# Optimization experiments

Measured on AMD Instinct MI355X. Metric: run time of the kernel, lower is better.

The kernel has to match this reference:

```python
import jax, jax.numpy as jnp
import numpy as np

WS = 7
NHEAD = 8


def setup_inputs() -> dict:
    key = jax.random.key(0)
    k1, k2, k3 = jax.random.split(key, 3)
    B, H, W, D = 32, 56, 56, 256
    x = jax.random.normal(k1, (B, H, W, D), dtype=jnp.float32)
    in_proj_w = jax.random.normal(k2, (3 * D, D), dtype=jnp.float32) * 0.02
    in_proj_b = jnp.zeros((3 * D,), dtype=jnp.float32)
    out_w = jax.random.normal(k3, (D, D), dtype=jnp.float32) * 0.02
    out_b = jnp.zeros((D,), dtype=jnp.float32)
    return {"x": x, "in_proj_w": in_proj_w, "in_proj_b": in_proj_b,
            "out_w": out_w, "out_b": out_b}


def reference(x, in_proj_w, in_proj_b, out_w, out_b):
    B, Hf, Wf, D = x.shape
    ws = WS
    hd = D // NHEAD
    pad_h = (-Hf) % ws
    pad_w = (-Wf) % ws
    xp = jnp.pad(x, ((0, 0), (0, pad_h), (0, pad_w), (0, 0)))
    Hp, Wp = Hf + pad_h, Wf + pad_w
    nh, nw = Hp // ws, Wp // ws
    # partition into windows: [B*nh*nw, ws*ws, D]
    xw = xp.reshape(B, nh, ws, nw, ws, D).transpose(0, 1, 3, 2, 4, 5)
    xw = xw.reshape(B * nh * nw, ws * ws, D)
    N, L = xw.shape[0], ws * ws
    # qkv projection (torch MHA: x @ in_proj_w.T + in_proj_b)
    qkv = jnp.einsum('nld,ed->nle', xw, in_proj_w) + in_proj_b  # [N, L, 3D]
    q, k, v = jnp.split(qkv, 3, axis=-1)
    q = q.reshape(N, L, NHEAD, hd).transpose(0, 2, 1, 3)
    k = k.reshape(N, L, NHEAD, hd).transpose(0, 2, 1, 3)
    v = v.reshape(N, L, NHEAD, hd).transpose(0, 2, 1, 3)
    scale = 1.0 / np.sqrt(hd).astype(np.float32)
    scores = jnp.einsum('nhqd,nhkd->nhqk', q * scale, k)  # [N, H, L, L]
    attn = jax.nn.softmax(scores, axis=-1)
    o = jnp.einsum('nhqk,nhkd->nhqd', attn, v)
    o = o.transpose(0, 2, 1, 3).reshape(N, L, D)
    o = jnp.einsum('nld,ed->nle', o, out_w) + out_b
    # un-window
    o = o.reshape(B, nh, nw, ws, ws, D).transpose(0, 1, 3, 2, 4, 5)
    o = o.reshape(B, Hp, Wp, D)
    return o[:, :Hf, :Wf, :]
```

## Files before the change

kernel.cpp:

```cpp
#include <hip/hip_runtime.h>


using f16   = _Float16;
using f16x4 = __attribute__((ext_vector_type(4))) _Float16;
using f16x8 = __attribute__((ext_vector_type(8))) _Float16;
using f32x4 = __attribute__((ext_vector_type(4))) float;

#define NTOK   100352
#define DMODEL 256
#define QKVN   768
#define QKV_BYTES 154140672ull
#define WQ_HALVES 196608
#define WO_HALVES 65536

typedef const __attribute__((address_space(1))) unsigned int* as1_u32p;
typedef __attribute__((address_space(3))) unsigned int* as3_u32p;

__device__ __forceinline__ void gload16(const void* g, void* l) {
    __builtin_amdgcn_global_load_lds((as1_u32p)g, (as3_u32p)l, 16, 0, 0);
}

__device__ __forceinline__ f16x8 zero8() {
    f16x8 z;
#pragma unroll
    for (int i = 0; i < 8; ++i) z[i] = (f16)0;
    return z;
}

#define WQV4  49152
#define WOV4  16384
__global__ __launch_bounds__(256) void convert_w(
    const float* __restrict__ Wq, const float* __restrict__ Wo,
    f16* __restrict__ Wqh, f16* __restrict__ Woh)
{
    const float scale = 0.17677669529663687f;
    int idx = blockIdx.x * blockDim.x + threadIdx.x;
    if (idx < WQV4) {
        int row = idx >> 6;
        float sc = (row < 256) ? scale : 1.0f;
        float4 f = reinterpret_cast<const float4*>(Wq)[idx];
        f16x4 h;
        h[0]=(f16)(f.x*sc); h[1]=(f16)(f.y*sc); h[2]=(f16)(f.z*sc); h[3]=(f16)(f.w*sc);
        reinterpret_cast<f16x4*>(Wqh)[idx] = h;
    } else if (Woh && idx < WQV4 + WOV4) {
        int j = idx - WQV4;
        float4 f = reinterpret_cast<const float4*>(Wo)[j];
        f16x4 h;
        h[0]=(f16)f.x; h[1]=(f16)f.y; h[2]=(f16)f.z; h[3]=(f16)f.w;
        reinterpret_cast<f16x4*>(Woh)[j] = h;
    }
}

__global__ __launch_bounds__(256) void qkv_gemm(
    const float* __restrict__ X,
    const f16* __restrict__ Wh,
    const float* __restrict__ bias,
    f16* __restrict__ QKV)
{
    __shared__ float As[128 * 64];
    __shared__ f16   Bs[128 * 64];
    const int tid  = threadIdx.x;
    const int lane = tid & 63;
    const int wave = tid >> 6;
    int wg = blockIdx.x;
    const int cpx = (NTOK / 128) * (QKVN / 128) / 8;
    wg = (wg & 7) * cpx + (wg >> 3);
    const int m0 = (wg / (QKVN / 128)) * 128;
    const int n0 = (wg % (QKVN / 128)) * 128;
    const int wm = (wave >> 1) * 64;
    const int wn = (wave & 1) * 64;
    const int g  = lane >> 4;
    const int lr = lane & 15;

    f32x4 acc[4][4] = {};

    for (int k0 = 0; k0 < 256; k0 += 64) {
#pragma unroll
        for (int j = 0; j < 8; ++j) {
            int s   = tid + j * 256;
            int row = s >> 4, c16 = s & 15;
            int cs  = c16 ^ (row & 15);
            gload16(X + (size_t)(m0 + row) * 256 + k0 + cs * 4, &As[s * 4]);
        }
#pragma unroll
        for (int j = 0; j < 4; ++j) {
            int s   = tid + j * 256;
            int row = s >> 3, sl = s & 7;
            int ss  = sl ^ (row & 7);
            gload16(Wh + (size_t)(n0 + row) * 256 + k0 + ss * 8, &Bs[s * 8]);
        }
        __syncthreads();
#pragma unroll
        for (int ks = 0; ks < 2; ++ks) {
            f16x8 a[4], b[4];
#pragma unroll
            for (int i = 0; i < 4; ++i) {
                int row = wm + i * 16 + lr;
                int t0  = (((ks << 2) + g) << 1);
                f32x4 lo = *reinterpret_cast<const f32x4*>(&As[row * 64 + (t0 ^ (row & 15)) * 4]);
                f32x4 hi = *reinterpret_cast<const f32x4*>(&As[row * 64 + ((t0 | 1) ^ (row & 15)) * 4]);
                f16x8 aa;
                aa[0]=(f16)lo[0]; aa[1]=(f16)lo[1]; aa[2]=(f16)lo[2]; aa[3]=(f16)lo[3];
                aa[4]=(f16)hi[0]; aa[5]=(f16)hi[1]; aa[6]=(f16)hi[2]; aa[7]=(f16)hi[3];
                a[i] = aa;
            }
#pragma unroll
            for (int i = 0; i < 4; ++i) {
                int row = wn + i * 16 + lr;
                int c   = ((ks << 2) + g) ^ (row & 7);
                b[i] = *reinterpret_cast<const f16x8*>(&Bs[row * 64 + c * 8]);
            }
#pragma unroll
            for (int mi = 0; mi < 4; ++mi)
#pragma unroll
                for (int ni = 0; ni < 4; ++ni)
                    acc[mi][ni] = __builtin_amdgcn_mfma_f32_16x16x32_f16(a[mi], b[ni], acc[mi][ni], 0, 0, 0);
        }
        __syncthreads();
    }
    const float scale = 0.17677669529663687f;
#pragma unroll
    for (int ni = 0; ni < 4; ++ni) {
        int n = n0 + wn + ni * 16 + lr;
        float bv = bias[n];
        if (n < 256) bv *= scale;
#pragma unroll
        for (int mi = 0; mi < 4; ++mi)
#pragma unroll
            for (int r = 0; r < 4; ++r) {
                int m = m0 + wm + mi * 16 + g * 4 + r;
                QKV[(size_t)m * QKVN + n] = (f16)(acc[mi][ni][r] + bv);
            }
    }
}

__global__ __launch_bounds__(256) void win_attn(f16* __restrict__ QKV)
{
    __shared__ f16 Vt[4][32][68];
    __shared__ f16 P[4][64][68];
    const int tid  = threadIdx.x;
    const int lane = tid & 63;
    const int w    = tid >> 6;
    const int u    = blockIdx.x * 4 + w;
    const int win = u >> 3, h = u & 7;
    const int b = win >> 6, wh = (win >> 3) & 7, ww = win & 7;
    const int base = (b * 56 + wh * 7) * 56 + ww * 7;
    const int g = lane >> 4, lr = lane & 15;

    auto tok = [&](int row) { int rr = row / 7; return base + rr * 56 + (row - rr * 7); };

    f16x8 qf[4], kf[4];
#pragma unroll
    for (int i = 0; i < 4; ++i) {
        int row = i * 16 + lr;
        if (row < 49) {
            size_t off = (size_t)tok(row) * QKVN + h * 32 + g * 8;
            qf[i] = *reinterpret_cast<const f16x8*>(QKV + off);
            kf[i] = *reinterpret_cast<const f16x8*>(QKV + off + 256);
        } else { qf[i] = zero8(); kf[i] = zero8(); }
    }
    {
        int kk = lane;
        if (kk < 49) {
            size_t off = (size_t)tok(kk) * QKVN + 512 + h * 32;
            f16x8 vv[4];
#pragma unroll
            for (int j = 0; j < 4; ++j)
                vv[j] = *reinterpret_cast<const f16x8*>(QKV + off + j * 8);
#pragma unroll
            for (int j = 0; j < 4; ++j)
#pragma unroll
                for (int d = 0; d < 8; ++d) Vt[w][j * 8 + d][kk] = vv[j][d];
        } else {
#pragma unroll
            for (int d = 0; d < 32; ++d) Vt[w][d][kk] = (f16)0;
        }
    }
    f32x4 s[4][4] = {};
#pragma unroll
    for (int ki = 0; ki < 4; ++ki)
#pragma unroll
        for (int qi = 0; qi < 4; ++qi)
            s[ki][qi] = __builtin_amdgcn_mfma_f32_16x16x32_f16(kf[ki], qf[qi], s[ki][qi], 0, 0, 0);

#pragma unroll
    for (int qi = 0; qi < 4; ++qi) {
        float e[4][4];
        float sum = 0.f;
#pragma unroll
        for (int ki = 0; ki < 4; ++ki)
#pragma unroll
            for (int r = 0; r < 4; ++r)
                e[ki][r] = __expf(s[ki][qi][r]);
#pragma unroll
        for (int ki = 0; ki < 3; ++ki)
#pragma unroll
            for (int r = 0; r < 4; ++r)
                sum += e[ki][r];
        sum += (g == 0) ? e[3][0] : 0.f;
        sum += __shfl_xor(sum, 16, 64);
        sum += __shfl_xor(sum, 32, 64);
        float is = 1.f / sum;
#pragma unroll
        for (int ki = 0; ki < 4; ++ki) {
            f16x4 pw;
            pw[0] = (f16)(e[ki][0] * is);
            pw[1] = (f16)(e[ki][1] * is);
            pw[2] = (f16)(e[ki][2] * is);
            pw[3] = (f16)(e[ki][3] * is);
            *reinterpret_cast<f16x4*>(&P[w][qi * 16 + lr][ki * 16 + g * 4]) = pw;
        }
    }
    __syncthreads();

    f32x4 o[4][2] = {};
#pragma unroll
    for (int ks = 0; ks < 2; ++ks) {
        f16x8 pa[4], vb[2];
#pragma unroll
        for (int mi = 0; mi < 4; ++mi)
            pa[mi] = *reinterpret_cast<const f16x8*>(&P[w][mi * 16 + lr][ks * 32 + g * 8]);
#pragma unroll
        for (int ni = 0; ni < 2; ++ni)
            vb[ni] = *reinterpret_cast<const f16x8*>(&Vt[w][ni * 16 + lr][ks * 32 + g * 8]);
#pragma unroll
        for (int mi = 0; mi < 4; ++mi)
#pragma unroll
            for (int ni = 0; ni < 2; ++ni)
                o[mi][ni] = __builtin_amdgcn_mfma_f32_16x16x32_f16(pa[mi], vb[ni], o[mi][ni], 0, 0, 0);
    }
#pragma unroll
    for (int mi = 0; mi < 4; ++mi)
#pragma unroll
        for (int r = 0; r < 4; ++r) {
            int row = mi * 16 + g * 4 + r;
            if (row < 49) {
                size_t off = (size_t)tok(row) * QKVN + h * 32;
#pragma unroll
                for (int ni = 0; ni < 2; ++ni)
                    QKV[off + ni * 16 + lr] = (f16)o[mi][ni][r];
            }
        }
}

__global__ __launch_bounds__(256) void out_gemm_f16(
    const f16* __restrict__ O,
    const f16* __restrict__ Wh,
    const float* __restrict__ bias,
    float* __restrict__ OUT)
{
    __shared__ f16 As[128 * 64];
    __shared__ f16 Bs[128 * 64];
    const int tid  = threadIdx.x;
    const int lane = tid & 63;
    const int wave = tid >> 6;
    int wg = blockIdx.x;
    const int cpx = (NTOK / 128) * (DMODEL / 128) / 8;
    wg = (wg & 7) * cpx + (wg >> 3);
    const int m0 = (wg / (DMODEL / 128)) * 128;
    const int n0 = (wg % (DMODEL / 128)) * 128;
    const int wm = (wave >> 1) * 64;
    const int wn = (wave & 1) * 64;
    const int g  = lane >> 4;
    const int lr = lane & 15;

    f32x4 acc[4][4] = {};

    for (int k0 = 0; k0 < 256; k0 += 64) {
#pragma unroll
        for (int j = 0; j < 4; ++j) {
            int s   = tid + j * 256;
            int row = s >> 3, sl = s & 7;
            int ss  = sl ^ (row & 7);
            gload16(O + (size_t)(m0 + row) * QKVN + k0 + ss * 8, &As[s * 8]);
        }
#pragma unroll
        for (int j = 0; j < 4; ++j) {
            int s   = tid + j * 256;
            int row = s >> 3, sl = s & 7;
            int ss  = sl ^ (row & 7);
            gload16(Wh + (size_t)(n0 + row) * 256 + k0 + ss * 8, &Bs[s * 8]);
        }
        __syncthreads();
#pragma unroll
        for (int ks = 0; ks < 2; ++ks) {
            f16x8 a[4], b[4];
#pragma unroll
            for (int i = 0; i < 4; ++i) {
                int row = wm + i * 16 + lr;
                int c   = ((ks << 2) + g) ^ (row & 7);
                a[i] = *reinterpret_cast<const f16x8*>(&As[row * 64 + c * 8]);
            }
#pragma unroll
            for (int i = 0; i < 4; ++i) {
                int row = wn + i * 16 + lr;
                int c   = ((ks << 2) + g) ^ (row & 7);
                b[i] = *reinterpret_cast<const f16x8*>(&Bs[row * 64 + c * 8]);
            }
#pragma unroll
            for (int mi = 0; mi < 4; ++mi)
#pragma unroll
                for (int ni = 0; ni < 4; ++ni)
                    acc[mi][ni] = __builtin_amdgcn_mfma_f32_16x16x32_f16(a[mi], b[ni], acc[mi][ni], 0, 0, 0);
        }
        __syncthreads();
    }
#pragma unroll
    for (int ni = 0; ni < 4; ++ni) {
        int n = n0 + wn + ni * 16 + lr;
        float bv = bias[n];
#pragma unroll
        for (int mi = 0; mi < 4; ++mi)
#pragma unroll
            for (int r = 0; r < 4; ++r) {
                int m = m0 + wm + mi * 16 + g * 4 + r;
                OUT[(size_t)m * 256 + n] = acc[mi][ni][r] + bv;
            }
    }
}

__global__ __launch_bounds__(256) void out_gemm_cvt(
    const f16* __restrict__ O,
    const float* __restrict__ W,
    const float* __restrict__ bias,
    float* __restrict__ OUT)
{
    __shared__ f16 As[128 * 64];
    __shared__ f16 Bs[128][72];
    const int tid  = threadIdx.x;
    const int lane = tid & 63;
    const int wave = tid >> 6;
    int wg = blockIdx.x;
    const int cpx = (NTOK / 128) * (DMODEL / 128) / 8;
    wg = (wg & 7) * cpx + (wg >> 3);
    const int m0 = (wg / (DMODEL / 128)) * 128;
    const int n0 = (wg % (DMODEL / 128)) * 128;
    const int wm = (wave >> 1) * 64;
    const int wn = (wave & 1) * 64;
    const int g  = lane >> 4;
    const int lr = lane & 15;

    f32x4 acc[4][4] = {};

    for (int k0 = 0; k0 < 256; k0 += 64) {
#pragma unroll
        for (int j = 0; j < 4; ++j) {
            int s   = tid + j * 256;
            int row = s >> 3, sl = s & 7;
            int ss  = sl ^ (row & 7);
            gload16(O + (size_t)(m0 + row) * QKVN + k0 + ss * 8, &As[s * 8]);
        }
#pragma unroll
        for (int j = 0; j < 8; ++j) {
            int v = tid + j * 256;
            int row = v >> 4, cv = v & 15;
            float4 f = *reinterpret_cast<const float4*>(W + (size_t)(n0 + row) * 256 + k0 + cv * 4);
            f16x4 h; h[0]=(f16)f.x; h[1]=(f16)f.y; h[2]=(f16)f.z; h[3]=(f16)f.w;
            *reinterpret_cast<f16x4*>(&Bs[row][cv * 4]) = h;
        }
        __syncthreads();
#pragma unroll
        for (int ks = 0; ks < 2; ++ks) {
            f16x8 a[4], b[4];
#pragma unroll
            for (int i = 0; i < 4; ++i) {
                int row = wm + i * 16 + lr;
                int c   = ((ks << 2) + g) ^ (row & 7);
                a[i] = *reinterpret_cast<const f16x8*>(&As[row * 64 + c * 8]);
            }
#pragma unroll
            for (int i = 0; i < 4; ++i)
                b[i] = *reinterpret_cast<const f16x8*>(&Bs[wn + i * 16 + lr][ks * 32 + g * 8]);
#pragma unroll
            for (int mi = 0; mi < 4; ++mi)
#pragma unroll
                for (int ni = 0; ni < 4; ++ni)
                    acc[mi][ni] = __builtin_amdgcn_mfma_f32_16x16x32_f16(a[mi], b[ni], acc[mi][ni], 0, 0, 0);
        }
        __syncthreads();
    }
#pragma unroll
    for (int ni = 0; ni < 4; ++ni) {
        int n = n0 + wn + ni * 16 + lr;
        float bv = bias[n];
#pragma unroll
        for (int mi = 0; mi < 4; ++mi)
#pragma unroll
            for (int r = 0; r < 4; ++r) {
                int m = m0 + wm + mi * 16 + g * 4 + r;
                OUT[(size_t)m * 256 + n] = acc[mi][ni][r] + bv;
            }
    }
}

extern "C" void kernel_launch(void* const* d_in, const int* in_sizes, int n_in,
                              void* d_out, int out_size, void* d_ws, size_t ws_size,
                              hipStream_t stream) {
    const float* x     = (const float*)d_in[0];
    const float* in_w  = (const float*)d_in[1];
    const float* in_b  = (const float*)d_in[2];
    const float* out_w = (const float*)d_in[3];
    const float* out_b = (const float*)d_in[4];
    float* out = (float*)d_out;
    f16* qkv = (f16*)d_ws;

    const bool tailok = ws_size >= QKV_BYTES + (size_t)(WQ_HALVES + WO_HALVES) * 2;
    f16* wqh = tailok ? (f16*)((char*)d_ws + QKV_BYTES) : (f16*)d_out;
    f16* woh = tailok ? wqh + WQ_HALVES : nullptr;

    convert_w<<<(WQV4 + WOV4 + 255) / 256, 256, 0, stream>>>(in_w, out_w, wqh, woh);

    qkv_gemm<<<(NTOK / 128) * (QKVN / 128), 256, 0, stream>>>(x, wqh, in_b, qkv);

    win_attn<<<4096, 256, 0, stream>>>(qkv);

    if (tailok)
        out_gemm_f16<<<(NTOK / 128) * (DMODEL / 128), 256, 0, stream>>>(qkv, woh, out_b, out);
    else
        out_gemm_cvt<<<(NTOK / 128) * (DMODEL / 128), 256, 0, stream>>>(qkv, out_w, out_b, out);
}
```

Before: 179.9 us.

## Pre-convert X to fp16 and double-buffer the QKV GEMM LDS tiles

Adds a grid-stride conversion kernel that writes X (plus both weight matrices) to fp16, staging X and the QKV weights in the output buffer as scratch. The QKV GEMM then loads fp16 A tiles with no per-fragment conversion and double-buffers its LDS stages so the next k-tile load overlaps the MFMAs. This halves A-tile LDS traffic and removes conversion work inside the GEMM loop. The cost is an extra full pass that reads X in fp32 and writes it back as fp16.

```diff
diff --git a/kernel.cpp b/kernel.cpp
--- a/kernel.cpp
+++ b/kernel.cpp
@@ -27,38 +27,48 @@
     return z;
 }
 
+#define XV4   6422528
 #define WQV4  49152
 #define WOV4  16384
-__global__ __launch_bounds__(256) void convert_w(
-    const float* __restrict__ Wq, const float* __restrict__ Wo,
-    f16* __restrict__ Wqh, f16* __restrict__ Woh)
+__global__ __launch_bounds__(256) void convert_all(
+    const float* __restrict__ X, const float* __restrict__ Wq,
+    const float* __restrict__ Wo,
+    f16* __restrict__ Xh, f16* __restrict__ Wqh, f16* __restrict__ Woh)
 {
     const float scale = 0.17677669529663687f;
-    int idx = blockIdx.x * blockDim.x + threadIdx.x;
-    if (idx < WQV4) {
-        int row = idx >> 6;
-        float sc = (row < 256) ? scale : 1.0f;
-        float4 f = reinterpret_cast<const float4*>(Wq)[idx];
+    const int total = XV4 + WQV4 + WOV4;
+    for (int i = blockIdx.x * blockDim.x + threadIdx.x; i < total;
+         i += gridDim.x * blockDim.x) {
+        float4 f;
         f16x4 h;
-        h[0]=(f16)(f.x*sc); h[1]=(f16)(f.y*sc); h[2]=(f16)(f.z*sc); h[3]=(f16)(f.w*sc);
-        reinterpret_cast<f16x4*>(Wqh)[idx] = h;
-    } else if (Woh && idx < WQV4 + WOV4) {
-        int j = idx - WQV4;
-        float4 f = reinterpret_cast<const float4*>(Wo)[j];
-        f16x4 h;
-        h[0]=(f16)f.x; h[1]=(f16)f.y; h[2]=(f16)f.z; h[3]=(f16)f.w;
-        reinterpret_cast<f16x4*>(Woh)[j] = h;
+        if (i < XV4) {
+            f = reinterpret_cast<const float4*>(X)[i];
+            h[0]=(f16)f.x; h[1]=(f16)f.y; h[2]=(f16)f.z; h[3]=(f16)f.w;
+            reinterpret_cast<f16x4*>(Xh)[i] = h;
+        } else if (i < XV4 + WQV4) {
+            int idx = i - XV4;
+            int row = idx >> 6;
+            float sc = (row < 256) ? scale : 1.0f;
+            f = reinterpret_cast<const float4*>(Wq)[idx];
+            h[0]=(f16)(f.x*sc); h[1]=(f16)(f.y*sc); h[2]=(f16)(f.z*sc); h[3]=(f16)(f.w*sc);
+            reinterpret_cast<f16x4*>(Wqh)[idx] = h;
+        } else if (Woh) {
+            int idx = i - XV4 - WQV4;
+            f = reinterpret_cast<const float4*>(Wo)[idx];
+            h[0]=(f16)f.x; h[1]=(f16)f.y; h[2]=(f16)f.z; h[3]=(f16)f.w;
+            reinterpret_cast<f16x4*>(Woh)[idx] = h;
+        }
     }
 }
 
 __global__ __launch_bounds__(256) void qkv_gemm(
-    const float* __restrict__ X,
+    const f16* __restrict__ Xh,
     const f16* __restrict__ Wh,
     const float* __restrict__ bias,
     f16* __restrict__ QKV)
 {
-    __shared__ float As[128 * 64];
-    __shared__ f16   Bs[128 * 64];
+    __shared__ f16 As[2][128 * 64];
+    __shared__ f16 Bs[2][128 * 64];
     const int tid  = threadIdx.x;
     const int lane = tid & 63;
     const int wave = tid >> 6;
@@ -72,43 +82,38 @@
     const int g  = lane >> 4;
     const int lr = lane & 15;
 
-    f32x4 acc[4][4] = {};
-
-    for (int k0 = 0; k0 < 256; k0 += 64) {
-#pragma unroll
-        for (int j = 0; j < 8; ++j) {
-            int s   = tid + j * 256;
-            int row = s >> 4, c16 = s & 15;
-            int cs  = c16 ^ (row & 15);
-            gload16(X + (size_t)(m0 + row) * 256 + k0 + cs * 4, &As[s * 4]);
-        }
+    auto stage = [&](int buf, int k0) {
 #pragma unroll
         for (int j = 0; j < 4; ++j) {
             int s   = tid + j * 256;
             int row = s >> 3, sl = s & 7;
             int ss  = sl ^ (row & 7);
-            gload16(Wh + (size_t)(n0 + row) * 256 + k0 + ss * 8, &Bs[s * 8]);
-        }
-        __syncthreads();
+            gload16(Xh + (size_t)(m0 + row) * 256 + k0 + ss * 8, &As[buf][s * 8]);
+            gload16(Wh + (size_t)(n0 + row) * 256 + k0 + ss * 8, &Bs[buf][s * 8]);
+        }
+    };
+
+    stage(0, 0);
+    __syncthreads();
+
+    f32x4 acc[4][4] = {};
+    int buf = 0;
+    for (int t = 0; t < 4; ++t) {
+        if (t < 3) stage(buf ^ 1, (t + 1) * 64);
 #pragma unroll
         for (int ks = 0; ks < 2; ++ks) {
             f16x8 a[4], b[4];
 #pragma unroll
             for (int i = 0; i < 4; ++i) {
                 int row = wm + i * 16 + lr;
-                int t0  = (((ks << 2) + g) << 1);
-                f32x4 lo = *reinterpret_cast<const f32x4*>(&As[row * 64 + (t0 ^ (row & 15)) * 4]);
-                f32x4 hi = *reinterpret_cast<const f32x4*>(&As[row * 64 + ((t0 | 1) ^ (row & 15)) * 4]);
-                f16x8 aa;
-                aa[0]=(f16)lo[0]; aa[1]=(f16)lo[1]; aa[2]=(f16)lo[2]; aa[3]=(f16)lo[3];
-                aa[4]=(f16)hi[0]; aa[5]=(f16)hi[1]; aa[6]=(f16)hi[2]; aa[7]=(f16)hi[3];
-                a[i] = aa;
+                int c   = ((ks << 2) + g) ^ (row & 7);
+                a[i] = *reinterpret_cast<const f16x8*>(&As[buf][row * 64 + c * 8]);
             }
 #pragma unroll
             for (int i = 0; i < 4; ++i) {
                 int row = wn + i * 16 + lr;
                 int c   = ((ks << 2) + g) ^ (row & 7);
-                b[i] = *reinterpret_cast<const f16x8*>(&Bs[row * 64 + c * 8]);
+                b[i] = *reinterpret_cast<const f16x8*>(&Bs[buf][row * 64 + c * 8]);
             }
 #pragma unroll
             for (int mi = 0; mi < 4; ++mi)
@@ -117,6 +122,7 @@
                     acc[mi][ni] = __builtin_amdgcn_mfma_f32_16x16x32_f16(a[mi], b[ni], acc[mi][ni], 0, 0, 0);
         }
         __syncthreads();
+        buf ^= 1;
     }
     const float scale = 0.17677669529663687f;
 #pragma unroll
@@ -273,12 +279,6 @@
             int row = s >> 3, sl = s & 7;
             int ss  = sl ^ (row & 7);
             gload16(O + (size_t)(m0 + row) * QKVN + k0 + ss * 8, &As[s * 8]);
-        }
-#pragma unroll
-        for (int j = 0; j < 4; ++j) {
-            int s   = tid + j * 256;
-            int row = s >> 3, sl = s & 7;
-            int ss  = sl ^ (row & 7);
             gload16(Wh + (size_t)(n0 + row) * 256 + k0 + ss * 8, &Bs[s * 8]);
         }
         __syncthreads();
@@ -404,13 +404,14 @@
     float* out = (float*)d_out;
     f16* qkv = (f16*)d_ws;
 
-    const bool tailok = ws_size >= QKV_BYTES + (size_t)(WQ_HALVES + WO_HALVES) * 2;
-    f16* wqh = tailok ? (f16*)((char*)d_ws + QKV_BYTES) : (f16*)d_out;
-    f16* woh = tailok ? wqh + WQ_HALVES : nullptr;
-
-    convert_w<<<(WQV4 + WOV4 + 255) / 256, 256, 0, stream>>>(in_w, out_w, wqh, woh);
-
-    qkv_gemm<<<(NTOK / 128) * (QKVN / 128), 256, 0, stream>>>(x, wqh, in_b, qkv);
+    f16* xh  = (f16*)d_out;
+    f16* wqh = xh + (size_t)NTOK * 256;
+    const bool tailok = ws_size >= QKV_BYTES + (size_t)WO_HALVES * 2;
+    f16* woh = tailok ? (f16*)((char*)d_ws + QKV_BYTES) : nullptr;
+
+    convert_all<<<2048, 256, 0, stream>>>(x, in_w, out_w, xh, wqh, woh);
+
+    qkv_gemm<<<(NTOK / 128) * (QKVN / 128), 256, 0, stream>>>(xh, wqh, in_b, qkv);
 
     win_attn<<<4096, 256, 0, stream>>>(qkv);
 
```

Measured after the change: 155.9 us. 13.4% less time.
